# Kernel optimization log

Hardware: AMD Instinct MI355X
Metric: run time of the kernel (lower is better)

The kernel has to match this reference:

```python
import jax, jax.numpy as jnp
import numpy as np

HEADS, MAX_SEQ, N_STATE = 8, 2048, 512
DEPTH = N_STATE // HEADS
B, S = 2, 2048
EPS = 1e-5


def setup_inputs() -> dict:
    key = jax.random.key(0)
    ks = jax.random.split(key, 8)
    sd = lambda f: 1.0 / np.sqrt(f)
    causal = jnp.tril(jnp.ones((S, S), dtype=bool))
    mask = jnp.where(causal, 0.0, -1e9).astype(jnp.float32)[None, None]
    return {
        "x": jax.random.normal(ks[0], (B, S, N_STATE), jnp.float32),
        "mask": mask,
        "W_qkv": jax.random.normal(ks[1], (N_STATE, 3 * N_STATE), jnp.float32) * sd(N_STATE),
        "b_qkv": jnp.zeros((3 * N_STATE,), jnp.float32),
        "W_proj": jax.random.normal(ks[2], (N_STATE, N_STATE), jnp.float32) * sd(N_STATE),
        "b_proj": jnp.zeros((N_STATE,), jnp.float32),
        "E": jax.random.normal(ks[3], (HEADS, MAX_SEQ, DEPTH), jnp.float32) * sd(DEPTH),
        "g1": jnp.ones((N_STATE,), jnp.float32),
        "be1": jnp.zeros((N_STATE,), jnp.float32),
        "g2": jnp.ones((N_STATE,), jnp.float32),
        "be2": jnp.zeros((N_STATE,), jnp.float32),
        "W_fc1": jax.random.normal(ks[4], (N_STATE, 4 * N_STATE), jnp.float32) * sd(N_STATE),
        "b_fc1": jnp.zeros((4 * N_STATE,), jnp.float32),
        "W_fc2": jax.random.normal(ks[5], (4 * N_STATE, N_STATE), jnp.float32) * sd(4 * N_STATE),
        "b_fc2": jnp.zeros((N_STATE,), jnp.float32),
    }


def _layernorm(x, g, b):
    mu = jnp.mean(x, axis=-1, keepdims=True)
    var = jnp.mean(jnp.square(x - mu), axis=-1, keepdims=True)
    return (x - mu) * jax.lax.rsqrt(var + EPS) * g + b


def _relative_skew(rel):
    # rel: [B, H, S, S] = q @ E_slice^T ; skew trick -> relative positions
    b, h, s, _ = rel.shape
    rel = jnp.pad(rel, ((0, 0), (0, 0), (0, 0), (1, 0)))  # [B,H,S,S+1]
    rel = rel.reshape(b, h, s + 1, s)
    return rel[:, :, 1:, :]  # [B,H,S,S]


def reference(x, mask, W_qkv, b_qkv, W_proj, b_proj, E, g1, be1, g2, be2,
              W_fc1, b_fc1, W_fc2, b_fc2):
    b, s, _ = x.shape
    a = _layernorm(x, g1, be1)
    qkv = a @ W_qkv + b_qkv  # [B,S,3N]
    q, k, v = jnp.split(qkv, 3, axis=-1)
    split = lambda t: t.reshape(b, s, HEADS, DEPTH).transpose(0, 2, 1, 3)  # [B,H,S,D]
    q, k, v = split(q), split(k), split(v)
    present = jnp.stack([k, v], axis=1)  # [B,2,H,S,D]

    w = jnp.einsum("bhqd,bhkd->bhqk", q, k)
    E_s = E[:, MAX_SEq if False else MAX_SEQ - s:, :]  # [H,S,D]
    rel = jnp.einsum("bhqd,hld->bhql", q, E_s)
    w = (w + _relative_skew(rel)) * (1.0 / np.sqrt(DEPTH))
    w = w + mask
    w = jax.nn.softmax(w, axis=-1)
    att = jnp.einsum("bhqk,bhkd->bhqd", w, v)
    att = att.transpose(0, 2, 1, 3).reshape(b, s, N_STATE)
    att = att @ W_proj + b_proj

    x = x + att
    m = _layernorm(x, g2, be2)
    m = jax.nn.gelu(m @ W_fc1 + b_fc1) @ W_fc2 + b_fc2
    x = x + m
    return (x, present)
```

## Files before the change

### kernel.cpp

```cpp
#include <hip/hip_runtime.h>
#include <stdint.h>

#define DEV __device__ __forceinline__
#define SCHEDB __builtin_amdgcn_sched_barrier(0)
#define WAITVM(n) asm volatile("s_waitcnt vmcnt(" #n ")" ::: "memory")
#define WAITLG asm volatile("s_waitcnt lgkmcnt(0)" ::: "memory")

typedef __attribute__((ext_vector_type(8))) short bf16x8;
typedef __attribute__((ext_vector_type(4))) float f32x4;

DEV ushort f2bf(float f) {
  union { float f; uint32_t u; } c; c.f = f;
  return (ushort)((c.u + 0x7FFFu + ((c.u >> 16) & 1)) >> 16);
}
DEV bf16x8 ld8(const ushort* p) { return *reinterpret_cast<const bf16x8*>(p); }

DEV void gload16(const void* g, void* l) {
  __builtin_amdgcn_global_load_lds(
      (const __attribute__((address_space(1))) uint32_t*)g,
      (__attribute__((address_space(3))) uint32_t*)l, 16, 0, 0);
}

__global__ __launch_bounds__(256) void k_transpose_bf(const float* __restrict__ in,
                                                      ushort* __restrict__ out,
                                                      int R, int C) {
  __shared__ float t[32][33];
  int tx = threadIdx.x & 31, ty = threadIdx.x >> 5;
  int c0 = blockIdx.x * 32, r0 = blockIdx.y * 32;
#pragma unroll
  for (int k = 0; k < 4; ++k)
    t[ty + 8 * k][tx] = in[(size_t)(r0 + ty + 8 * k) * C + c0 + tx];
  __syncthreads();
#pragma unroll
  for (int k = 0; k < 4; ++k)
    out[(size_t)(c0 + ty + 8 * k) * R + r0 + tx] = f2bf(t[tx][ty + 8 * k]);
}

__global__ __launch_bounds__(256) void k_cvt_bf(const float* __restrict__ in,
                                                ushort* __restrict__ out, int n4) {
  int i = blockIdx.x * 256 + threadIdx.x;
  if (i >= n4) return;
  float4 v = reinterpret_cast<const float4*>(in)[i];
  ushort4 o; o.x = f2bf(v.x); o.y = f2bf(v.y); o.z = f2bf(v.z); o.w = f2bf(v.w);
  reinterpret_cast<ushort4*>(out)[i] = o;
}

__global__ __launch_bounds__(256) void k_ln(const float* __restrict__ x,
                                            const float* __restrict__ g,
                                            const float* __restrict__ be,
                                            ushort* __restrict__ out) {
  int w = threadIdx.x >> 6, lane = threadIdx.x & 63;
  int row = blockIdx.x * 4 + w;
  const float* xr = x + (size_t)row * 512 + lane * 8;
  float4 a = *reinterpret_cast<const float4*>(xr);
  float4 b = *reinterpret_cast<const float4*>(xr + 4);
  float xs[8] = {a.x, a.y, a.z, a.w, b.x, b.y, b.z, b.w};
  float s = 0.f, q = 0.f;
#pragma unroll
  for (int i = 0; i < 8; ++i) { s += xs[i]; q += xs[i] * xs[i]; }
#pragma unroll
  for (int off = 32; off; off >>= 1) { s += __shfl_xor(s, off); q += __shfl_xor(q, off); }
  float mu = s * (1.f / 512.f);
  float var = q * (1.f / 512.f) - mu * mu;
  float inv = rsqrtf(var + 1e-5f);
  const float* gp = g + lane * 8;
  const float* bp = be + lane * 8;
  ushort o[8];
#pragma unroll
  for (int i = 0; i < 8; ++i) o[i] = f2bf((xs[i] - mu) * inv * gp[i] + bp[i]);
  *reinterpret_cast<uint4*>(out + (size_t)row * 512 + lane * 8) = *reinterpret_cast<uint4*>(o);
}

template <int EPI, int BN>
__global__ __launch_bounds__(256) void k_gemm(
    const ushort* __restrict__ A, const ushort* __restrict__ Bt,
    int M, int N, int K,
    const float* __restrict__ bias, const float* __restrict__ res,
    float* __restrict__ outf, ushort* __restrict__ outb,
    float* __restrict__ present, ushort* __restrict__ qbf,
    ushort* __restrict__ kbf, ushort* __restrict__ vtbf) {
  constexpr int NF = BN / 32;
  __shared__ ushort As[2][128][64];
  __shared__ ushort Bs[2][BN][64];
  const int tid = threadIdx.x, lane = tid & 63, w = tid >> 6;
  const int g = lane >> 4, l16 = lane & 15;
  const int m0 = blockIdx.y * 128, n0 = blockIdx.x * BN;
  const int wm = (w >> 1) * 64, wn = (w & 1) * (BN / 2);
  f32x4 acc[4][NF];
#pragma unroll
  for (int i = 0; i < 4; ++i)
#pragma unroll
    for (int j = 0; j < NF; ++j) acc[i][j] = (f32x4){0.f, 0.f, 0.f, 0.f};

  auto stage = [&](int buf, int k0) {
#pragma unroll
    for (int sw = 0; sw < 4; ++sw) {
      int chunk = sw * 4 + w;
      int row = chunk * 8 + (lane >> 3);
      int ccp = (lane & 7) ^ (row & 7);
      gload16((const char*)A + (((size_t)(m0 + row) * K + k0) << 1) + (ccp << 4),
              (char*)(&As[buf][0][0]) + chunk * 1024);
    }
#pragma unroll
    for (int sw = 0; sw < BN / 32; ++sw) {
      int chunk = sw * 4 + w;
      int row = chunk * 8 + (lane >> 3);
      int ccp = (lane & 7) ^ (row & 7);
      gload16((const char*)Bt + (((size_t)(n0 + row) * K + k0) << 1) + (ccp << 4),
              (char*)(&Bs[buf][0][0]) + chunk * 1024);
    }
  };

  const int nt = K >> 6;
  stage(0, 0);
  stage(1, 64);
  if constexpr (BN == 128) WAITVM(8); else WAITVM(6);
  SCHEDB;
  __builtin_amdgcn_s_barrier();
  SCHEDB;

  const char* AsB0 = (const char*)&As[0][0][0];
  const char* BsB0 = (const char*)&Bs[0][0][0];
  for (int t = 0; t < nt; ++t) {
    const int cur = t & 1;
    const char* AsB = AsB0 + cur * (128 * 128);
    const char* BsB = BsB0 + cur * (BN * 128);
    bf16x8 af[2][4], bfr[2][NF];
#pragma unroll
    for (int kk = 0; kk < 2; ++kk) {
#pragma unroll
      for (int f = 0; f < 4; ++f) {
        int row = wm + f * 16 + l16;
        af[kk][f] = ld8((const ushort*)(AsB + row * 128 + (((kk * 4 + g) ^ (row & 7)) << 4)));
      }
#pragma unroll
      for (int f = 0; f < NF; ++f) {
        int row = wn + f * 16 + l16;
        bfr[kk][f] = ld8((const ushort*)(BsB + row * 128 + (((kk * 4 + g) ^ (row & 7)) << 4)));
      }
    }
    WAITLG;
    SCHEDB;
    __builtin_amdgcn_s_barrier();
    SCHEDB;
    if (t + 2 < nt) stage(cur, (t + 2) << 6);
    SCHEDB;
#pragma unroll
    for (int kk = 0; kk < 2; ++kk)
#pragma unroll
      for (int i = 0; i < 4; ++i)
#pragma unroll
        for (int j = 0; j < NF; ++j)
          acc[i][j] = __builtin_amdgcn_mfma_f32_16x16x32_bf16(
              af[kk][i], bfr[kk][j], acc[i][j], 0, 0, 0);
    SCHEDB;
    if (t + 1 < nt) {
      if (t + 2 < nt) {
        if constexpr (BN == 128) WAITVM(8); else WAITVM(6);
      } else {
        WAITVM(0);
      }
      SCHEDB;
      __builtin_amdgcn_s_barrier();
      SCHEDB;
    }
  }

#pragma unroll
  for (int i = 0; i < 4; ++i)
#pragma unroll
    for (int j = 0; j < NF; ++j)
#pragma unroll
      for (int r = 0; r < 4; ++r) {
        int row = m0 + wm + i * 16 + g * 4 + r;
        int col = n0 + wn + j * 16 + l16;
        float v = acc[i][j][r] + bias[col];
        if constexpr (EPI == 0) {
          int third = col >> 9, hh = (col >> 6) & 7, d = col & 63;
          int bb = row >> 11, sq = row & 2047;
          if (third == 0) {
            qbf[((((size_t)bb * 8 + hh) * 2048) + sq) * 64 + d] = f2bf(v);
          } else {
            present[((((size_t)bb * 2 + (third - 1)) * 8 + hh) * 2048 + sq) * 64 + d] = v;
            if (third == 1)
              kbf[((((size_t)bb * 8 + hh) * 2048) + sq) * 64 + d] = f2bf(v);
            else
              vtbf[(((size_t)bb * 8 + hh) * 64 + d) * 2048 + sq] = f2bf(v);
          }
        } else if constexpr (EPI == 1) {
          size_t idx = (size_t)row * N + col;
          outf[idx] = v + res[idx];
        } else {
          float u = 0.7978845608f * (v + 0.044715f * v * v * v);
          float e = __expf(2.f * u);
          float th = 1.f - 2.f / (e + 1.f);
          outb[(size_t)row * N + col] = f2bf(0.5f * v * (1.f + th));
        }
      }
}

__global__ __launch_bounds__(256, 2) void k_attn(
    const ushort* __restrict__ qbf, const ushort* __restrict__ kbf,
    const ushort* __restrict__ vtbf, const ushort* __restrict__ Ebf,
    ushort* __restrict__ attb) {
  constexpr int S = 2048;
  __shared__ ushort Ks[2][64][64];
  __shared__ ushort Vs[2][64][64];
  __shared__ ushort Es[2][128][64];
  __shared__ ushort Ps[4][16][76];
  const int tid = threadIdx.x, lane = tid & 63, w = tid >> 6;
  const int g = lane >> 4, l16 = lane & 15;
  const int bid = blockIdx.x;
  const int h = bid & 7, rest = bid >> 3;
  const int b = rest & 1;
  const int tq = (rest < 32) ? (31 - (rest >> 1)) : ((rest - 32) >> 1);
  const int bh = b * 8 + h;

  const ushort* qp = qbf + (size_t)bh * S * 64;
  const ushort* kp = kbf + (size_t)bh * S * 64;
  const ushort* vp = vtbf + (size_t)bh * 64 * S;
  const ushort* ep = Ebf + (size_t)h * S * 64;

  const int i0 = tq * 64;
  const int iw = i0 + w * 16;
  const int rbase = 48 - w * 16;

  bf16x8 qf[2];
  qf[0] = ld8(qp + (size_t)(iw + l16) * 64 + g * 8);
  qf[1] = ld8(qp + (size_t)(iw + l16) * 64 + 32 + g * 8);
  f32x4 o[4];
#pragma unroll
  for (int fv = 0; fv < 4; ++fv) o[fv] = (f32x4){0.f, 0.f, 0.f, 0.f};
  float mrun[4], lrun[4];
#pragma unroll
  for (int r = 0; r < 4; ++r) { mrun[r] = -1e30f; lrun[r] = 0.f; }
  const int nkt = tq + 1;

  auto stage = [&](int buf, int kt) {
    const int j0 = kt * 64;
    const int ebase = S - 64 - i0 + j0;
#pragma unroll
    for (int c = 0; c < 2; ++c) {
      int chunk = w * 2 + c;
      int row = chunk * 8 + (lane >> 3);
      int ccp = (lane & 7) ^ (row & 7);
      gload16(kp + (size_t)(j0 + row) * 64 + ccp * 8,
              (char*)(&Ks[buf][0][0]) + chunk * 1024);
      gload16(vp + (size_t)row * S + j0 + ccp * 8,
              (char*)(&Vs[buf][0][0]) + chunk * 1024);
    }
#pragma unroll
    for (int c = 0; c < 4; ++c) {
      int chunk = w * 4 + c;
      int row = chunk * 8 + (lane >> 3);
      int l = ebase + row;
      l = l < 0 ? 0 : (l > S - 1 ? S - 1 : l);
      int ccp = (lane & 7) ^ (row & 7);
      gload16(ep + (size_t)l * 64 + ccp * 8,
              (char*)(&Es[buf][0][0]) + chunk * 1024);
    }
  };

  stage(0, 0);
  WAITVM(0);
  SCHEDB;
  __builtin_amdgcn_s_barrier();
  SCHEDB;

  for (int kt = 0; kt < nkt; ++kt) {
    const int cur = kt & 1;
    const int j0 = kt * 64;
    if (kt + 1 < nkt) stage(cur ^ 1, kt + 1);
    SCHEDB;
    const char* KsB = (const char*)&Ks[cur][0][0];
    const char* VsB = (const char*)&Vs[cur][0][0];
    const char* EsB = (const char*)&Es[cur][0][0];

    f32x4 sacc[4];
#pragma unroll
    for (int fn = 0; fn < 4; ++fn) sacc[fn] = (f32x4){0.f, 0.f, 0.f, 0.f};
#pragma unroll
    for (int kk = 0; kk < 2; ++kk)
#pragma unroll
      for (int fn = 0; fn < 4; ++fn) {
        int row = fn * 16 + l16, chunk = kk * 4 + g;
        bf16x8 kfr = ld8((const ushort*)(KsB + row * 128 + (((chunk ^ (row & 7))) << 4)));
        sacc[fn] = __builtin_amdgcn_mfma_f32_16x16x32_bf16(qf[kk], kfr, sacc[fn], 0, 0, 0);
      }
    f32x4 racc[5];
#pragma unroll
    for (int fc = 0; fc < 5; ++fc) racc[fc] = (f32x4){0.f, 0.f, 0.f, 0.f};
#pragma unroll
    for (int kk = 0; kk < 2; ++kk)
#pragma unroll
      for (int fc = 0; fc < 5; ++fc) {
        int row = rbase + fc * 16 + l16, chunk = kk * 4 + g;
        bf16x8 efr = ld8((const ushort*)(EsB + row * 128 + (((chunk ^ (row & 7))) << 4)));
        racc[fc] = __builtin_amdgcn_mfma_f32_16x16x32_bf16(qf[kk], efr, racc[fc], 0, 0, 0);
      }

    float Sv[4][4], mtile[4];
#pragma unroll
    for (int r = 0; r < 4; ++r) mtile[r] = -1e30f;
#pragma unroll
    for (int r = 0; r < 4; ++r) {
      const int dr = g * 4 + r;
      const int src = (lane & 48) | ((l16 + 15 - dr) & 15);
      const bool hi = (l16 > dr);
#pragma unroll
      for (int fn = 0; fn < 4; ++fn) {
        float lo_v = __shfl(racc[fn][r], src);
        float hi_v = __shfl(racc[fn + 1][r], src);
        float rel = hi ? hi_v : lo_v;
        float sv = (sacc[fn][r] + rel) * 0.125f;
        int dj = fn * 16 + l16;
        if (j0 + dj > iw + dr) sv = -1e30f;
        Sv[fn][r] = sv;
        mtile[r] = fmaxf(mtile[r], sv);
      }
    }
#pragma unroll
    for (int off = 1; off < 16; off <<= 1)
#pragma unroll
      for (int r = 0; r < 4; ++r) mtile[r] = fmaxf(mtile[r], __shfl_xor(mtile[r], off));
    float corr[4], psum[4];
#pragma unroll
    for (int r = 0; r < 4; ++r) {
      float mn = fmaxf(mrun[r], mtile[r]);
      corr[r] = __expf(mrun[r] - mn);
      mrun[r] = mn;
      psum[r] = 0.f;
    }
#pragma unroll
    for (int fn = 0; fn < 4; ++fn)
#pragma unroll
      for (int r = 0; r < 4; ++r) {
        float pv = __expf(Sv[fn][r] - mrun[r]);
        psum[r] += pv;
        Ps[w][g * 4 + r][fn * 16 + l16] = f2bf(pv);
      }
#pragma unroll
    for (int off = 1; off < 16; off <<= 1)
#pragma unroll
      for (int r = 0; r < 4; ++r) psum[r] += __shfl_xor(psum[r], off);
#pragma unroll
    for (int r = 0; r < 4; ++r) lrun[r] = lrun[r] * corr[r] + psum[r];
#pragma unroll
    for (int fv = 0; fv < 4; ++fv)
#pragma unroll
      for (int r = 0; r < 4; ++r) o[fv][r] *= corr[r];

#pragma unroll
    for (int kk = 0; kk < 2; ++kk) {
      bf16x8 pf = ld8(&Ps[w][l16][kk * 32 + g * 8]);
#pragma unroll
      for (int fv = 0; fv < 4; ++fv) {
        int row = fv * 16 + l16, chunk = kk * 4 + g;
        bf16x8 vfr = ld8((const ushort*)(VsB + row * 128 + (((chunk ^ (row & 7))) << 4)));
        o[fv] = __builtin_amdgcn_mfma_f32_16x16x32_bf16(pf, vfr, o[fv], 0, 0, 0);
      }
    }
    SCHEDB;
    if (kt + 1 < nkt) {
      WAITVM(0);
      SCHEDB;
      __builtin_amdgcn_s_barrier();
      SCHEDB;
    }
  }

#pragma unroll
  for (int fv = 0; fv < 4; ++fv)
#pragma unroll
    for (int r = 0; r < 4; ++r) {
      int dr = g * 4 + r;
      float v = o[fv][r] / lrun[r];
      attb[(size_t)(b * S + iw + dr) * 512 + h * 64 + fv * 16 + l16] = f2bf(v);
    }
}

extern "C" void kernel_launch(void* const* d_in, const int* in_sizes, int n_in,
                              void* d_out, int out_size, void* d_ws, size_t ws_size,
                              hipStream_t stream) {
  const float* x = (const float*)d_in[0];
  const float* W_qkv = (const float*)d_in[2];
  const float* b_qkv = (const float*)d_in[3];
  const float* W_proj = (const float*)d_in[4];
  const float* b_proj = (const float*)d_in[5];
  const float* E = (const float*)d_in[6];
  const float* g1 = (const float*)d_in[7];
  const float* be1 = (const float*)d_in[8];
  const float* g2 = (const float*)d_in[9];
  const float* be2 = (const float*)d_in[10];
  const float* W_fc1 = (const float*)d_in[11];
  const float* b_fc1 = (const float*)d_in[12];
  const float* W_fc2 = (const float*)d_in[13];
  const float* b_fc2 = (const float*)d_in[14];

  float* x_out = (float*)d_out;
  float* present = x_out + 2097152;

  char* ws = (char*)d_ws;
  ushort* a_bf   = (ushort*)(ws + 0);
  ushort* m_bf   = (ushort*)(ws + 4194304);
  ushort* q_bf   = (ushort*)(ws + 8388608);
  ushort* att_bf = (ushort*)(ws + 12582912);
  ushort* h_bf   = (ushort*)(ws + 16777216);
  ushort* k_bf   = (ushort*)(ws + 16777216);
  ushort* vt_bf  = (ushort*)(ws + 20971520);
  float*  x2     = (float*)(ws + 33554432);
  ushort* Wqkv_t = (ushort*)(ws + 41943040);
  ushort* Wproj_t= (ushort*)(ws + 43515904);
  ushort* Wfc1_t = (ushort*)(ws + 44040192);
  ushort* Wfc2_t = (ushort*)(ws + 46137344);
  ushort* E_bf   = (ushort*)(ws + 48234496);

  k_transpose_bf<<<dim3(48, 16), 256, 0, stream>>>(W_qkv, Wqkv_t, 512, 1536);
  k_transpose_bf<<<dim3(16, 16), 256, 0, stream>>>(W_proj, Wproj_t, 512, 512);
  k_transpose_bf<<<dim3(64, 16), 256, 0, stream>>>(W_fc1, Wfc1_t, 512, 2048);
  k_transpose_bf<<<dim3(16, 64), 256, 0, stream>>>(W_fc2, Wfc2_t, 2048, 512);
  k_cvt_bf<<<1024, 256, 0, stream>>>(E, E_bf, 262144);
  k_ln<<<1024, 256, 0, stream>>>(x, g1, be1, a_bf);
  k_gemm<0, 128><<<dim3(12, 32), 256, 0, stream>>>(a_bf, Wqkv_t, 4096, 1536, 512,
                                                   b_qkv, nullptr, nullptr, nullptr,
                                                   present, q_bf, k_bf, vt_bf);
  k_attn<<<512, 256, 0, stream>>>(q_bf, k_bf, vt_bf, E_bf, att_bf);
  k_gemm<1, 64><<<dim3(8, 32), 256, 0, stream>>>(att_bf, Wproj_t, 4096, 512, 512,
                                                 b_proj, x, x2, nullptr, nullptr, nullptr,
                                                 nullptr, nullptr);
  k_ln<<<1024, 256, 0, stream>>>(x2, g2, be2, m_bf);
  k_gemm<2, 128><<<dim3(16, 32), 256, 0, stream>>>(m_bf, Wfc1_t, 4096, 2048, 512,
                                                   b_fc1, nullptr, nullptr, h_bf, nullptr,
                                                   nullptr, nullptr, nullptr);
  k_gemm<1, 64><<<dim3(8, 32), 256, 0, stream>>>(h_bf, Wfc2_t, 4096, 512, 2048,
                                                 b_fc2, x2, x_out, nullptr, nullptr, nullptr,
                                                 nullptr, nullptr);
}
```

Baseline: 273.2 us.

## Use two-wave attention blocks with 32 query rows per wave sharing K/E fragments

Cuts the attention block from four waves to two, with each wave handling two 16-row query sub-tiles. K and V fragments read from LDS, and a shared set of six E fragments, are reused across both sub-tiles, which lowers LDS read traffic per MFMA. Each wave now issues twice as many global-to-LDS staging loads, and per-thread register use grows because of the doubled accumulators. That may reduce occupancy and leaves fewer waves per block to hide latency. The lower clamp on the E row index is dropped, presumably because it cannot go negative.

```diff
diff --git a/kernel.cpp b/kernel.cpp
--- a/kernel.cpp
+++ b/kernel.cpp
@@ -199,7 +199,7 @@
       }
 }
 
-__global__ __launch_bounds__(256, 2) void k_attn(
+__global__ __launch_bounds__(128, 2) void k_attn(
     const ushort* __restrict__ qbf, const ushort* __restrict__ kbf,
     const ushort* __restrict__ vtbf, const ushort* __restrict__ Ebf,
     ushort* __restrict__ attb) {
@@ -207,7 +207,7 @@
   __shared__ ushort Ks[2][64][64];
   __shared__ ushort Vs[2][64][64];
   __shared__ ushort Es[2][128][64];
-  __shared__ ushort Ps[4][16][76];
+  __shared__ ushort Ps[2][32][72];
   const int tid = threadIdx.x, lane = tid & 63, w = tid >> 6;
   const int g = lane >> 4, l16 = lane & 15;
   const int bid = blockIdx.x;
@@ -222,26 +222,33 @@
   const ushort* ep = Ebf + (size_t)h * S * 64;
 
   const int i0 = tq * 64;
-  const int iw = i0 + w * 16;
-  const int rbase = 48 - w * 16;
-
-  bf16x8 qf[2];
-  qf[0] = ld8(qp + (size_t)(iw + l16) * 64 + g * 8);
-  qf[1] = ld8(qp + (size_t)(iw + l16) * 64 + 32 + g * 8);
-  f32x4 o[4];
-#pragma unroll
-  for (int fv = 0; fv < 4; ++fv) o[fv] = (f32x4){0.f, 0.f, 0.f, 0.f};
-  float mrun[4], lrun[4];
-#pragma unroll
-  for (int r = 0; r < 4; ++r) { mrun[r] = -1e30f; lrun[r] = 0.f; }
+  const int iw = i0 + w * 32;
+  const int efb = 32 - 32 * w;
+
+  bf16x8 qf[2][2];
+#pragma unroll
+  for (int h2 = 0; h2 < 2; ++h2) {
+    qf[h2][0] = ld8(qp + (size_t)(iw + 16 * h2 + l16) * 64 + g * 8);
+    qf[h2][1] = ld8(qp + (size_t)(iw + 16 * h2 + l16) * 64 + 32 + g * 8);
+  }
+  f32x4 o[2][4];
+#pragma unroll
+  for (int h2 = 0; h2 < 2; ++h2)
+#pragma unroll
+    for (int fv = 0; fv < 4; ++fv) o[h2][fv] = (f32x4){0.f, 0.f, 0.f, 0.f};
+  float mrun[2][4], lrun[2][4];
+#pragma unroll
+  for (int h2 = 0; h2 < 2; ++h2)
+#pragma unroll
+    for (int r = 0; r < 4; ++r) { mrun[h2][r] = -1e30f; lrun[h2][r] = 0.f; }
   const int nkt = tq + 1;
 
   auto stage = [&](int buf, int kt) {
     const int j0 = kt * 64;
     const int ebase = S - 64 - i0 + j0;
 #pragma unroll
-    for (int c = 0; c < 2; ++c) {
-      int chunk = w * 2 + c;
+    for (int c = 0; c < 4; ++c) {
+      int chunk = w * 4 + c;
       int row = chunk * 8 + (lane >> 3);
       int ccp = (lane & 7) ^ (row & 7);
       gload16(kp + (size_t)(j0 + row) * 64 + ccp * 8,
@@ -250,11 +257,11 @@
               (char*)(&Vs[buf][0][0]) + chunk * 1024);
     }
 #pragma unroll
-    for (int c = 0; c < 4; ++c) {
-      int chunk = w * 4 + c;
+    for (int c = 0; c < 8; ++c) {
+      int chunk = w * 8 + c;
       int row = chunk * 8 + (lane >> 3);
       int l = ebase + row;
-      l = l < 0 ? 0 : (l > S - 1 ? S - 1 : l);
+      if (l > S - 1) l = S - 1;
       int ccp = (lane & 7) ^ (row & 7);
       gload16(ep + (size_t)l * 64 + ccp * 8,
               (char*)(&Es[buf][0][0]) + chunk * 1024);
@@ -276,88 +283,106 @@
     const char* VsB = (const char*)&Vs[cur][0][0];
     const char* EsB = (const char*)&Es[cur][0][0];
 
-    f32x4 sacc[4];
-#pragma unroll
-    for (int fn = 0; fn < 4; ++fn) sacc[fn] = (f32x4){0.f, 0.f, 0.f, 0.f};
+    f32x4 sacc[2][4];
+#pragma unroll
+    for (int h2 = 0; h2 < 2; ++h2)
+#pragma unroll
+      for (int fn = 0; fn < 4; ++fn) sacc[h2][fn] = (f32x4){0.f, 0.f, 0.f, 0.f};
 #pragma unroll
     for (int kk = 0; kk < 2; ++kk)
 #pragma unroll
       for (int fn = 0; fn < 4; ++fn) {
         int row = fn * 16 + l16, chunk = kk * 4 + g;
-        bf16x8 kfr = ld8((const ushort*)(KsB + row * 128 + (((chunk ^ (row & 7))) << 4)));
-        sacc[fn] = __builtin_amdgcn_mfma_f32_16x16x32_bf16(qf[kk], kfr, sacc[fn], 0, 0, 0);
-      }
-    f32x4 racc[5];
-#pragma unroll
-    for (int fc = 0; fc < 5; ++fc) racc[fc] = (f32x4){0.f, 0.f, 0.f, 0.f};
+        bf16x8 kfr = ld8((const ushort*)(KsB + row * 128 + ((chunk ^ (row & 7)) << 4)));
+        sacc[0][fn] = __builtin_amdgcn_mfma_f32_16x16x32_bf16(qf[0][kk], kfr, sacc[0][fn], 0, 0, 0);
+        sacc[1][fn] = __builtin_amdgcn_mfma_f32_16x16x32_bf16(qf[1][kk], kfr, sacc[1][fn], 0, 0, 0);
+      }
+    bf16x8 ef[2][6];
 #pragma unroll
     for (int kk = 0; kk < 2; ++kk)
 #pragma unroll
+      for (int f = 0; f < 6; ++f) {
+        int row = efb + f * 16 + l16, chunk = kk * 4 + g;
+        ef[kk][f] = ld8((const ushort*)(EsB + row * 128 + ((chunk ^ (row & 7)) << 4)));
+      }
+    f32x4 racc[2][5];
+#pragma unroll
+    for (int h2 = 0; h2 < 2; ++h2)
+#pragma unroll
+      for (int fc = 0; fc < 5; ++fc) racc[h2][fc] = (f32x4){0.f, 0.f, 0.f, 0.f};
+#pragma unroll
+    for (int kk = 0; kk < 2; ++kk)
+#pragma unroll
       for (int fc = 0; fc < 5; ++fc) {
-        int row = rbase + fc * 16 + l16, chunk = kk * 4 + g;
-        bf16x8 efr = ld8((const ushort*)(EsB + row * 128 + (((chunk ^ (row & 7))) << 4)));
-        racc[fc] = __builtin_amdgcn_mfma_f32_16x16x32_bf16(qf[kk], efr, racc[fc], 0, 0, 0);
-      }
-
-    float Sv[4][4], mtile[4];
-#pragma unroll
-    for (int r = 0; r < 4; ++r) mtile[r] = -1e30f;
-#pragma unroll
-    for (int r = 0; r < 4; ++r) {
-      const int dr = g * 4 + r;
-      const int src = (lane & 48) | ((l16 + 15 - dr) & 15);
-      const bool hi = (l16 > dr);
-#pragma unroll
-      for (int fn = 0; fn < 4; ++fn) {
-        float lo_v = __shfl(racc[fn][r], src);
-        float hi_v = __shfl(racc[fn + 1][r], src);
-        float rel = hi ? hi_v : lo_v;
-        float sv = (sacc[fn][r] + rel) * 0.125f;
-        int dj = fn * 16 + l16;
-        if (j0 + dj > iw + dr) sv = -1e30f;
-        Sv[fn][r] = sv;
-        mtile[r] = fmaxf(mtile[r], sv);
-      }
-    }
-#pragma unroll
-    for (int off = 1; off < 16; off <<= 1)
-#pragma unroll
-      for (int r = 0; r < 4; ++r) mtile[r] = fmaxf(mtile[r], __shfl_xor(mtile[r], off));
-    float corr[4], psum[4];
-#pragma unroll
-    for (int r = 0; r < 4; ++r) {
-      float mn = fmaxf(mrun[r], mtile[r]);
-      corr[r] = __expf(mrun[r] - mn);
-      mrun[r] = mn;
-      psum[r] = 0.f;
-    }
-#pragma unroll
-    for (int fn = 0; fn < 4; ++fn)
+        racc[0][fc] = __builtin_amdgcn_mfma_f32_16x16x32_bf16(qf[0][kk], ef[kk][fc + 1], racc[0][fc], 0, 0, 0);
+        racc[1][fc] = __builtin_amdgcn_mfma_f32_16x16x32_bf16(qf[1][kk], ef[kk][fc], racc[1][fc], 0, 0, 0);
+      }
+
+#pragma unroll
+    for (int h2 = 0; h2 < 2; ++h2) {
+      const int ih = iw + 16 * h2;
+      float Sv[4][4], mtile[4];
+#pragma unroll
+      for (int r = 0; r < 4; ++r) mtile[r] = -1e30f;
 #pragma unroll
       for (int r = 0; r < 4; ++r) {
-        float pv = __expf(Sv[fn][r] - mrun[r]);
-        psum[r] += pv;
-        Ps[w][g * 4 + r][fn * 16 + l16] = f2bf(pv);
-      }
-#pragma unroll
-    for (int off = 1; off < 16; off <<= 1)
-#pragma unroll
-      for (int r = 0; r < 4; ++r) psum[r] += __shfl_xor(psum[r], off);
-#pragma unroll
-    for (int r = 0; r < 4; ++r) lrun[r] = lrun[r] * corr[r] + psum[r];
-#pragma unroll
-    for (int fv = 0; fv < 4; ++fv)
-#pragma unroll
-      for (int r = 0; r < 4; ++r) o[fv][r] *= corr[r];
+        const int dr = g * 4 + r;
+        const int src = (lane & 48) | ((l16 + 15 - dr) & 15);
+        const bool hi = (l16 > dr);
+#pragma unroll
+        for (int fn = 0; fn < 4; ++fn) {
+          float lo_v = __shfl(racc[h2][fn][r], src);
+          float hi_v = __shfl(racc[h2][fn + 1][r], src);
+          float rel = hi ? hi_v : lo_v;
+          float sv = (sacc[h2][fn][r] + rel) * 0.125f;
+          int dj = fn * 16 + l16;
+          if (j0 + dj > ih + dr) sv = -1e30f;
+          Sv[fn][r] = sv;
+          mtile[r] = fmaxf(mtile[r], sv);
+        }
+      }
+#pragma unroll
+      for (int off = 1; off < 16; off <<= 1)
+#pragma unroll
+        for (int r = 0; r < 4; ++r) mtile[r] = fmaxf(mtile[r], __shfl_xor(mtile[r], off));
+      float corr[4], psum[4];
+#pragma unroll
+      for (int r = 0; r < 4; ++r) {
+        float mn = fmaxf(mrun[h2][r], mtile[r]);
+        corr[r] = __expf(mrun[h2][r] - mn);
+        mrun[h2][r] = mn;
+        psum[r] = 0.f;
+      }
+#pragma unroll
+      for (int fn = 0; fn < 4; ++fn)
+#pragma unroll
+        for (int r = 0; r < 4; ++r) {
+          float pv = __expf(Sv[fn][r] - mrun[h2][r]);
+          psum[r] += pv;
+          Ps[w][h2 * 16 + g * 4 + r][fn * 16 + l16] = f2bf(pv);
+        }
+#pragma unroll
+      for (int off = 1; off < 16; off <<= 1)
+#pragma unroll
+        for (int r = 0; r < 4; ++r) psum[r] += __shfl_xor(psum[r], off);
+#pragma unroll
+      for (int r = 0; r < 4; ++r) lrun[h2][r] = lrun[h2][r] * corr[r] + psum[r];
+#pragma unroll
+      for (int fv = 0; fv < 4; ++fv)
+#pragma unroll
+        for (int r = 0; r < 4; ++r) o[h2][fv][r] *= corr[r];
+    }
 
 #pragma unroll
     for (int kk = 0; kk < 2; ++kk) {
-      bf16x8 pf = ld8(&Ps[w][l16][kk * 32 + g * 8]);
+      bf16x8 pf0 = ld8(&Ps[w][l16][kk * 32 + g * 8]);
+      bf16x8 pf1 = ld8(&Ps[w][16 + l16][kk * 32 + g * 8]);
 #pragma unroll
       for (int fv = 0; fv < 4; ++fv) {
         int row = fv * 16 + l16, chunk = kk * 4 + g;
-        bf16x8 vfr = ld8((const ushort*)(VsB + row * 128 + (((chunk ^ (row & 7))) << 4)));
-        o[fv] = __builtin_amdgcn_mfma_f32_16x16x32_bf16(pf, vfr, o[fv], 0, 0, 0);
+        bf16x8 vfr = ld8((const ushort*)(VsB + row * 128 + ((chunk ^ (row & 7)) << 4)));
+        o[0][fv] = __builtin_amdgcn_mfma_f32_16x16x32_bf16(pf0, vfr, o[0][fv], 0, 0, 0);
+        o[1][fv] = __builtin_amdgcn_mfma_f32_16x16x32_bf16(pf1, vfr, o[1][fv], 0, 0, 0);
       }
     }
     SCHEDB;
@@ -370,13 +395,15 @@
   }
 
 #pragma unroll
-  for (int fv = 0; fv < 4; ++fv)
-#pragma unroll
-    for (int r = 0; r < 4; ++r) {
-      int dr = g * 4 + r;
-      float v = o[fv][r] / lrun[r];
-      attb[(size_t)(b * S + iw + dr) * 512 + h * 64 + fv * 16 + l16] = f2bf(v);
-    }
+  for (int h2 = 0; h2 < 2; ++h2)
+#pragma unroll
+    for (int fv = 0; fv < 4; ++fv)
+#pragma unroll
+      for (int r = 0; r < 4; ++r) {
+        int dr = g * 4 + r;
+        float v = o[h2][fv][r] / lrun[h2][r];
+        attb[(size_t)(b * S + iw + 16 * h2 + dr) * 512 + h * 64 + fv * 16 + l16] = f2bf(v);
+      }
 }
 
 extern "C" void kernel_launch(void* const* d_in, const int* in_sizes, int n_in,
@@ -424,7 +451,7 @@
   k_gemm<0, 128><<<dim3(12, 32), 256, 0, stream>>>(a_bf, Wqkv_t, 4096, 1536, 512,
                                                    b_qkv, nullptr, nullptr, nullptr,
                                                    present, q_bf, k_bf, vt_bf);
-  k_attn<<<512, 256, 0, stream>>>(q_bf, k_bf, vt_bf, E_bf, att_bf);
+  k_attn<<<512, 128, 0, stream>>>(q_bf, k_bf, vt_bf, E_bf, att_bf);
   k_gemm<1, 64><<<dim3(8, 32), 256, 0, stream>>>(att_bf, Wproj_t, 4096, 512, 512,
                                                  b_proj, x, x2, nullptr, nullptr, nullptr,
                                                  nullptr, nullptr);
```

Measured after the change: 309.7 us. 13.3% more time.
